# Performance work log

Measured on AMD Instinct MI355X. Metric: run time of the kernel, lower is better.

The kernel has to match this reference:

```python
import jax, jax.numpy as jnp
import numpy as np

B, S, HID = 2, 2048, 2048
NH, HD = 16, 128
QR, KR, VR = 6, 2, 2
SCALING = HD ** -0.5


def _rope_factors(x, cos, sin):
    # x: [b, s, rank, hd]; cos/sin: [s, hd//2]
    half = x.shape[-1] // 2
    x1, x2 = x[..., :half], x[..., half:]
    c = cos[None, :, None, :]
    s = sin[None, :, None, :]
    return jnp.concatenate([x1 * c - x2 * s, x1 * s + x2 * c], axis=-1)


def setup_inputs() -> dict:
    key = jax.random.key(0)
    ks = jax.random.split(key, 9)
    hidden_states = jax.random.normal(ks[0], (B, S, HID), dtype=jnp.float32)
    # proper RoPE frequencies
    inv_freq = 1.0 / (10000.0 ** (np.arange(0, HD, 2, dtype=np.float32) / HD))
    ang = np.arange(S, dtype=np.float32)[:, None] * inv_freq[None, :]  # [S, HD//2]
    freqs_cos = jnp.asarray(np.cos(ang), dtype=jnp.float32)
    freqs_sin = jnp.asarray(np.sin(ang), dtype=jnp.float32)
    kv_write_indices = jnp.arange(S, dtype=jnp.int64 if jax.config.jax_enable_x64 else jnp.int32)
    mask = jnp.zeros((B, 1, S, S), dtype=jnp.float32)
    sc = 0.02
    W_A_q = jax.random.normal(ks[1], (NH * QR, HID), dtype=jnp.float32) * sc
    W_A_k = jax.random.normal(ks[2], (NH * KR, HID), dtype=jnp.float32) * sc
    W_A_v = jax.random.normal(ks[3], (NH * VR, HID), dtype=jnp.float32) * sc
    W_B_q = jax.random.normal(ks[4], (QR * HD, HID), dtype=jnp.float32) * sc
    W_B_k = jax.random.normal(ks[5], (KR * HD, HID), dtype=jnp.float32) * sc
    W_B_v = jax.random.normal(ks[6], (VR * HD, HID), dtype=jnp.float32) * sc
    W_o = jax.random.normal(ks[7], (HID, NH * HD), dtype=jnp.float32) * sc
    return dict(hidden_states=hidden_states, freqs_cos=freqs_cos, freqs_sin=freqs_sin,
                kv_write_indices=kv_write_indices, mask=mask,
                W_A_q=W_A_q, W_A_k=W_A_k, W_A_v=W_A_v,
                W_B_q=W_B_q, W_B_k=W_B_k, W_B_v=W_B_v, W_o=W_o)


def reference(hidden_states, freqs_cos, freqs_sin, kv_write_indices, mask,
              W_A_q, W_A_k, W_A_v, W_B_q, W_B_k, W_B_v, W_o):
    b, s, _ = hidden_states.shape
    x = hidden_states
    # low-rank factor projections (torch Linear: x @ W.T)
    A_q = (x @ W_A_q.T).reshape(b, s, NH, QR)
    A_k = (x @ W_A_k.T).reshape(b, s, NH, KR)
    A_v = (x @ W_A_v.T).reshape(b, s, NH, VR)
    B_q = (x @ W_B_q.T).reshape(b, s, QR, HD)
    B_k = (x @ W_B_k.T).reshape(b, s, KR, HD)
    B_v = (x @ W_B_v.T).reshape(b, s, VR, HD)
    # per-rank RoPE on B factors of q and k (vectorized over rank)
    B_q = _rope_factors(B_q, freqs_cos, freqs_sin)
    B_k = _rope_factors(B_k, freqs_cos, freqs_sin)
    # kv_write_indices == arange(s): cache is fully overwritten, so current
    # activations are the full KV state (prefill).
    # reconstruct q/k/v from factor pairs
    q = jnp.einsum('bshr,bsrd->bshd', A_q, B_q) / QR
    k = jnp.einsum('bshr,bsrd->bshd', A_k, B_k) / KR
    v = jnp.einsum('bshr,bsrd->bshd', A_v, B_v) / VR
    # attention: [b, h, q, k]
    scores = jnp.einsum('bqhd,bkhd->bhqk', q * SCALING, k)
    scores = scores + mask
    probs = jax.nn.softmax(scores.astype(jnp.float32), axis=-1).astype(q.dtype)
    out = jnp.einsum('bhqk,bkhd->bqhd', probs, v).reshape(b, s, NH * HD)
    return out @ W_o.T
```

## Files before the change

### kernel.cpp

```cpp
#include <hip/hip_runtime.h>


typedef __attribute__((ext_vector_type(8))) __bf16 bf16x8;
typedef __attribute__((ext_vector_type(4))) float f32x4;

__device__ __forceinline__ unsigned short f2bf(float f) {
  union { float f; unsigned u; } v; v.f = f;
  unsigned u = v.u;
  u += 0x7fffu + ((u >> 16) & 1u);
  return (unsigned short)(u >> 16);
}

__device__ __forceinline__ void glds16(const void* g, void* l) {
  __builtin_amdgcn_global_load_lds(
      (const __attribute__((address_space(1))) void*)g,
      (__attribute__((address_space(3))) void*)l, 16, 0, 0);
}

__global__ void cast_bf16_k(const float* __restrict__ src,
                            unsigned short* __restrict__ dst, int n4) {
  int i = blockIdx.x * 256 + threadIdx.x;
  if (i < n4) {
    float4 f = reinterpret_cast<const float4*>(src)[i];
    ushort4 o;
    o.x = f2bf(f.x); o.y = f2bf(f.y); o.z = f2bf(f.z); o.w = f2bf(f.w);
    reinterpret_cast<ushort4*>(dst)[i] = o;
  }
}

__global__ __launch_bounds__(256, 2) void gemm_bt(
    const unsigned short* __restrict__ A, const unsigned short* __restrict__ Bt,
    float* __restrict__ C, int M, int N, int K) {
  __shared__ __align__(16) unsigned short As[128 * 32];
  __shared__ __align__(16) unsigned short Bs[128 * 32];
  const int tid = threadIdx.x;
  const int lane = tid & 63, wave = tid >> 6;
  const int l15 = lane & 15, quad = lane >> 4;
  const long bm = (long)blockIdx.y * 128, bn = (long)blockIdx.x * 128;
  const int wm = (wave >> 1) * 64, wn = (wave & 1) * 64;
  const f32x4 zero4 = {0.f, 0.f, 0.f, 0.f};
  f32x4 acc[4][4];
#pragma unroll
  for (int i = 0; i < 4; i++)
#pragma unroll
    for (int j = 0; j < 4; j++) acc[i][j] = zero4;

  const int g0 = tid, g1 = tid + 256;
  for (int k0 = 0; k0 < K; k0 += 32) {
    glds16(A + (bm + (g0 >> 2)) * K + k0 + (g0 & 3) * 8, As + g0 * 8);
    glds16(A + (bm + (g1 >> 2)) * K + k0 + (g1 & 3) * 8, As + g1 * 8);
    glds16(Bt + (bn + (g0 >> 2)) * K + k0 + (g0 & 3) * 8, Bs + g0 * 8);
    glds16(Bt + (bn + (g1 >> 2)) * K + k0 + (g1 & 3) * 8, Bs + g1 * 8);
    __syncthreads();
    bf16x8 af[4], bfr[4];
#pragma unroll
    for (int mi = 0; mi < 4; mi++)
      af[mi] = *(const bf16x8*)(As + (wm + mi * 16 + l15) * 32 + quad * 8);
#pragma unroll
    for (int ni = 0; ni < 4; ni++)
      bfr[ni] = *(const bf16x8*)(Bs + (wn + ni * 16 + l15) * 32 + quad * 8);
#pragma unroll
    for (int mi = 0; mi < 4; mi++)
#pragma unroll
      for (int ni = 0; ni < 4; ni++)
        acc[mi][ni] = __builtin_amdgcn_mfma_f32_16x16x32_bf16(
            af[mi], bfr[ni], acc[mi][ni], 0, 0, 0);
    __syncthreads();
  }
#pragma unroll
  for (int mi = 0; mi < 4; mi++)
#pragma unroll
    for (int ni = 0; ni < 4; ni++)
#pragma unroll
      for (int e = 0; e < 4; e++) {
        long r = bm + wm + mi * 16 + quad * 4 + e;
        long c = bn + wn + ni * 16 + l15;
        C[r * (long)N + c] = acc[mi][ni][e];
      }
}

__global__ __launch_bounds__(256) void rope_contract(
    const float* __restrict__ P, const float* __restrict__ cos_t,
    const float* __restrict__ sin_t, unsigned short* __restrict__ qo,
    unsigned short* __restrict__ ko, unsigned short* __restrict__ vo) {
  const int row = blockIdx.x;
  const int b = row >> 11, s = row & 2047;
  const float* p = P + (size_t)row * 1536;
  __shared__ float Af[160];
  __shared__ float Bqr[768], Bkr[256], Bvr[256];
  const int tid = threadIdx.x;
  if (tid < 160) Af[tid] = p[tid];
  for (int i = tid; i < 768; i += 256) {
    int r = i >> 7, d = i & 127;
    float out;
    if (d < 64) {
      float x1 = p[160 + r * 128 + d], x2 = p[160 + r * 128 + d + 64];
      out = x1 * cos_t[s * 64 + d] - x2 * sin_t[s * 64 + d];
    } else {
      int dd = d - 64;
      float x1 = p[160 + r * 128 + dd], x2 = p[160 + r * 128 + d];
      out = x1 * sin_t[s * 64 + dd] + x2 * cos_t[s * 64 + dd];
    }
    Bqr[i] = out;
  }
  {
    int i = tid;
    int r = i >> 7, d = i & 127;
    float out;
    if (d < 64) {
      float x1 = p[928 + r * 128 + d], x2 = p[928 + r * 128 + d + 64];
      out = x1 * cos_t[s * 64 + d] - x2 * sin_t[s * 64 + d];
    } else {
      int dd = d - 64;
      float x1 = p[928 + r * 128 + dd], x2 = p[928 + r * 128 + d];
      out = x1 * sin_t[s * 64 + dd] + x2 * cos_t[s * 64 + dd];
    }
    Bkr[i] = out;
    Bvr[i] = p[1184 + i];
  }
  __syncthreads();
  const float qscale = 0.08838834764831845f / 6.0f * 1.4426950408889634f;
  for (int i = tid; i < 2048; i += 256) {
    int h = i >> 7, d = i & 127;
    float aq = 0.f;
#pragma unroll
    for (int r = 0; r < 6; r++) aq += Af[h * 6 + r] * Bqr[r * 128 + d];
    float ak = Af[96 + h * 2] * Bkr[d] + Af[96 + h * 2 + 1] * Bkr[128 + d];
    float av = Af[128 + h * 2] * Bvr[d] + Af[128 + h * 2 + 1] * Bvr[128 + d];
    size_t o = ((size_t)(b * 16 + h) * 2048 + s) * 128 + d;
    qo[o] = f2bf(aq * qscale);
    ko[o] = f2bf(ak * 0.5f);
    vo[o] = f2bf(av * 0.5f);
  }
}

__global__ void transpose_v(const unsigned short* __restrict__ v,
                            unsigned short* __restrict__ vT) {
  __shared__ unsigned short t[32][33];
  const int bh = blockIdx.z, d0 = blockIdx.x * 32, s0 = blockIdx.y * 32;
  const int tx = threadIdx.x & 31, ty = threadIdx.x >> 5;
  const unsigned short* src = v + (size_t)bh * 2048 * 128;
  unsigned short* dst = vT + (size_t)bh * 128 * 2048;
#pragma unroll
  for (int j = 0; j < 32; j += 8)
    t[ty + j][tx] = src[(size_t)(s0 + ty + j) * 128 + d0 + tx];
  __syncthreads();
#pragma unroll
  for (int j = 0; j < 32; j += 8)
    dst[(size_t)(d0 + ty + j) * 2048 + s0 + tx] = t[tx][ty + j];
}

__global__ __launch_bounds__(512, 2) void attn_k(
    const unsigned short* __restrict__ q, const unsigned short* __restrict__ k,
    const unsigned short* __restrict__ vT, unsigned short* __restrict__ O) {
  const int bh = blockIdx.y;
  const int b = bh >> 4, h = bh & 15;
  const int q0 = blockIdx.x * 256;
  const int tid = threadIdx.x, wave = tid >> 6, lane = tid & 63;
  const int l15 = lane & 15, quad = lane >> 4;
  __shared__ __align__(16) unsigned short Kb[2][64 * 128];
  __shared__ __align__(16) unsigned short Vb[2][128 * 64];
  __shared__ __align__(16) unsigned short Ps[8][32 * 40];
  unsigned short* pw = &Ps[wave][0];
  const f32x4 zero4 = {0.f, 0.f, 0.f, 0.f};

  bf16x8 qf[2][4];
  {
    const unsigned short* qbase =
        q + ((size_t)bh * 2048 + q0 + wave * 32) * 128;
#pragma unroll
    for (int mi = 0; mi < 2; mi++)
#pragma unroll
      for (int ks = 0; ks < 4; ks++)
        qf[mi][ks] = *(const bf16x8*)(qbase + (size_t)(mi * 16 + l15) * 128 +
                                      ks * 32 + quad * 8);
  }
  bf16x8 ones;
#pragma unroll
  for (int i = 0; i < 8; i++) ones[i] = (__bf16)1.0f;

  f32x4 oacc[2][9];
#pragma unroll
  for (int mi = 0; mi < 2; mi++)
#pragma unroll
    for (int nd = 0; nd < 9; nd++) oacc[mi][nd] = zero4;

  const unsigned short* kg[2];
  const unsigned short* vg[2];
#pragma unroll
  for (int j = 0; j < 2; j++) {
    int t = tid + j * 512;
    int r = t >> 4, cb = (t & 15) ^ (r & 15);
    kg[j] = k + ((size_t)bh * 2048 + r) * 128 + cb * 8;
    int d = t >> 3, cv = (t & 7) ^ (d & 7);
    vg[j] = vT + ((size_t)bh * 128 + d) * 2048 + cv * 8;
  }

#define STAGE(KT, BUF)                                                        \
  {                                                                           \
    _Pragma("unroll") for (int j = 0; j < 2; j++) {                           \
      glds16(kg[j] + (size_t)(KT) * 128, &Kb[BUF][(tid + j * 512) * 8]);      \
      glds16(vg[j] + (KT), &Vb[BUF][(tid + j * 512) * 8]);                    \
    }                                                                         \
  }

  STAGE(0, 0);
  for (int it = 0; it < 32; it++) {
    __syncthreads();
    if (it + 1 < 32) STAGE((it + 1) * 64, (it + 1) & 1);
    const unsigned short* Kt = &Kb[it & 1][0];
    const unsigned short* Vt = &Vb[it & 1][0];

#pragma unroll
    for (int half = 0; half < 2; half++) {
      f32x4 sacc[2][2];
#pragma unroll
      for (int mi = 0; mi < 2; mi++) { sacc[mi][0] = zero4; sacc[mi][1] = zero4; }
#pragma unroll
      for (int ks = 0; ks < 4; ks++) {
        bf16x8 b0 = *(const bf16x8*)(
            Kt + (size_t)(half * 32 + l15) * 128 + (((ks * 4 + quad) ^ l15) * 8));
        bf16x8 b1 = *(const bf16x8*)(
            Kt + (size_t)(half * 32 + 16 + l15) * 128 + (((ks * 4 + quad) ^ l15) * 8));
#pragma unroll
        for (int mi = 0; mi < 2; mi++) {
          sacc[mi][0] = __builtin_amdgcn_mfma_f32_16x16x32_bf16(
              qf[mi][ks], b0, sacc[mi][0], 0, 0, 0);
          sacc[mi][1] = __builtin_amdgcn_mfma_f32_16x16x32_bf16(
              qf[mi][ks], b1, sacc[mi][1], 0, 0, 0);
        }
      }
#pragma unroll
      for (int mi = 0; mi < 2; mi++)
#pragma unroll
        for (int ni = 0; ni < 2; ni++)
#pragma unroll
          for (int e = 0; e < 4; e++) {
            float pv = __builtin_exp2f(sacc[mi][ni][e]);
            pw[(mi * 16 + quad * 4 + e) * 40 + ni * 16 + l15] =
                (unsigned short)(__float_as_uint(pv) >> 16);
          }
      bf16x8 bv[8];
#pragma unroll
      for (int nd = 0; nd < 8; nd++)
        bv[nd] = *(const bf16x8*)(
            Vt + (size_t)(nd * 16 + l15) * 64 + (((half * 4 + quad) ^ (l15 & 7)) * 8));
#pragma unroll
      for (int mi = 0; mi < 2; mi++) {
        bf16x8 af = *(const bf16x8*)(pw + (size_t)(mi * 16 + l15) * 40 + quad * 8);
#pragma unroll
        for (int nd = 0; nd < 8; nd++)
          oacc[mi][nd] = __builtin_amdgcn_mfma_f32_16x16x32_bf16(
              af, bv[nd], oacc[mi][nd], 0, 0, 0);
        oacc[mi][8] = __builtin_amdgcn_mfma_f32_16x16x32_bf16(
            af, ones, oacc[mi][8], 0, 0, 0);
      }
    }
  }

#pragma unroll
  for (int mi = 0; mi < 2; mi++)
#pragma unroll
    for (int e = 0; e < 4; e++) {
      float rl = 1.0f / oacc[mi][8][e];
      int srow = q0 + wave * 32 + mi * 16 + quad * 4 + e;
      size_t obase = ((size_t)b * 2048 + srow) * 2048 + h * 128;
#pragma unroll
      for (int nd = 0; nd < 8; nd++)
        O[obase + nd * 16 + l15] = f2bf(oacc[mi][nd][e] * rl);
    }
#undef STAGE
}

extern "C" void kernel_launch(void* const* d_in, const int* in_sizes, int n_in,
                              void* d_out, int out_size, void* d_ws, size_t ws_size,
                              hipStream_t stream) {
  const float* x   = (const float*)d_in[0];
  const float* fc  = (const float*)d_in[1];
  const float* fs  = (const float*)d_in[2];
  const float* WAq = (const float*)d_in[5];
  const float* WAk = (const float*)d_in[6];
  const float* WAv = (const float*)d_in[7];
  const float* WBq = (const float*)d_in[8];
  const float* WBk = (const float*)d_in[9];
  const float* WBv = (const float*)d_in[10];
  const float* Wo  = (const float*)d_in[11];
  float* out = (float*)d_out;
  char* ws = (char*)d_ws;

  unsigned short* Xbf  = (unsigned short*)(ws);
  unsigned short* Wcat = (unsigned short*)(ws + 16777216);
  unsigned short* Wob  = (unsigned short*)(ws + 23068672);
  float*          P    = (float*)(ws + 31457280);
  unsigned short* qb   = (unsigned short*)(ws + 56623104);
  unsigned short* kb   = (unsigned short*)(ws + 73400320);
  unsigned short* vb   = (unsigned short*)(ws + 90177536);
  unsigned short* vT   = Xbf;
  unsigned short* Ob   = (unsigned short*)P;

  auto cast = [&](const float* s, unsigned short* d, int n) {
    int n4 = n >> 2;
    cast_bf16_k<<<(n4 + 255) / 256, 256, 0, stream>>>(s, d, n4);
  };
  cast(x,   Xbf,               2 * 2048 * 2048);
  cast(WAq, Wcat + 0 * 2048,   96 * 2048);
  cast(WAk, Wcat + 96 * 2048,  32 * 2048);
  cast(WAv, Wcat + 128 * 2048, 32 * 2048);
  cast(WBq, Wcat + 160 * 2048, 768 * 2048);
  cast(WBk, Wcat + 928 * 2048, 256 * 2048);
  cast(WBv, Wcat + 1184 * 2048, 256 * 2048);
  cast(Wo,  Wob,               2048 * 2048);
  hipMemsetAsync(Wcat + 1440 * 2048, 0, (1536 - 1440) * 2048 * sizeof(unsigned short), stream);

  gemm_bt<<<dim3(12, 32), 256, 0, stream>>>(Xbf, Wcat, P, 4096, 1536, 2048);
  rope_contract<<<4096, 256, 0, stream>>>(P, fc, fs, qb, kb, vb);
  transpose_v<<<dim3(4, 64, 32), 256, 0, stream>>>(vb, vT);
  attn_k<<<dim3(8, 32), 512, 0, stream>>>(qb, kb, vT, Ob);
  gemm_bt<<<dim3(16, 32), 256, 0, stream>>>(Ob, Wob, out, 4096, 2048, 2048);
}
```

Baseline: 368.7 us.

## Fuse casts into one kernel and retile attention to 128-row blocks

Folds the eight cast launches and the memset into one kernel that picks its source and destination by index range, removing launch overhead. The attention kernel moves to 256-thread blocks covering 128 query rows, which doubles the grid to 512 blocks for better CU fill on 256 CUs. Block IDs are swizzled so that consecutive blocks go to different (b,h) pairs, and s_setprio raises wave priority around the MFMA sections. Smaller blocks mean each block re-stages the full K/V for fewer queries, so total K/V load traffic grows.

Result: faster. 344.7 us (-6.5%).

```diff
diff --git a/kernel.cpp b/kernel.cpp
--- a/kernel.cpp
+++ b/kernel.cpp
@@ -17,15 +17,32 @@
       (__attribute__((address_space(3))) void*)l, 16, 0, 0);
 }
 
-__global__ void cast_bf16_k(const float* __restrict__ src,
-                            unsigned short* __restrict__ dst, int n4) {
+__global__ __launch_bounds__(256) void cast_all_k(
+    const float* __restrict__ x, const float* __restrict__ WAq,
+    const float* __restrict__ WAk, const float* __restrict__ WAv,
+    const float* __restrict__ WBq, const float* __restrict__ WBk,
+    const float* __restrict__ WBv, const float* __restrict__ Wo,
+    unsigned short* __restrict__ Xbf, unsigned short* __restrict__ Wcat,
+    unsigned short* __restrict__ Wob) {
   int i = blockIdx.x * 256 + threadIdx.x;
-  if (i < n4) {
-    float4 f = reinterpret_cast<const float4*>(src)[i];
-    ushort4 o;
-    o.x = f2bf(f.x); o.y = f2bf(f.y); o.z = f2bf(f.z); o.w = f2bf(f.w);
-    reinterpret_cast<ushort4*>(dst)[i] = o;
-  }
+  const float* src; unsigned short* dst; int r;
+  if (i < 2097152)      { src = x;   dst = Xbf;               r = i; }
+  else if (i < 2146304) { src = WAq; dst = Wcat;              r = i - 2097152; }
+  else if (i < 2162688) { src = WAk; dst = Wcat + 96 * 2048;  r = i - 2146304; }
+  else if (i < 2179072) { src = WAv; dst = Wcat + 128 * 2048; r = i - 2162688; }
+  else if (i < 2572288) { src = WBq; dst = Wcat + 160 * 2048; r = i - 2179072; }
+  else if (i < 2703360) { src = WBk; dst = Wcat + 928 * 2048; r = i - 2572288; }
+  else if (i < 2834432) { src = WBv; dst = Wcat + 1184 * 2048; r = i - 2703360; }
+  else if (i < 3883008) { src = Wo;  dst = Wob;               r = i - 2834432; }
+  else {
+    ushort4 z = {0, 0, 0, 0};
+    reinterpret_cast<ushort4*>(Wcat + 1440 * 2048)[i - 3883008] = z;
+    return;
+  }
+  float4 f = reinterpret_cast<const float4*>(src)[r];
+  ushort4 o;
+  o.x = f2bf(f.x); o.y = f2bf(f.y); o.z = f2bf(f.z); o.w = f2bf(f.w);
+  reinterpret_cast<ushort4*>(dst)[r] = o;
 }
 
 __global__ __launch_bounds__(256, 2) void gemm_bt(
@@ -150,17 +167,19 @@
     dst[(size_t)(d0 + ty + j) * 2048 + s0 + tx] = t[tx][ty + j];
 }
 
-__global__ __launch_bounds__(512, 2) void attn_k(
+__global__ __launch_bounds__(256, 2) void attn_k(
     const unsigned short* __restrict__ q, const unsigned short* __restrict__ k,
     const unsigned short* __restrict__ vT, unsigned short* __restrict__ O) {
-  const int bh = blockIdx.y;
+  const int orig = blockIdx.y * 16 + blockIdx.x;
+  const int swz = (orig & 7) * 64 + (orig >> 3);
+  const int bh = swz >> 4;
   const int b = bh >> 4, h = bh & 15;
-  const int q0 = blockIdx.x * 256;
+  const int q0 = (swz & 15) * 128;
   const int tid = threadIdx.x, wave = tid >> 6, lane = tid & 63;
   const int l15 = lane & 15, quad = lane >> 4;
   __shared__ __align__(16) unsigned short Kb[2][64 * 128];
   __shared__ __align__(16) unsigned short Vb[2][128 * 64];
-  __shared__ __align__(16) unsigned short Ps[8][32 * 40];
+  __shared__ __align__(16) unsigned short Ps[4][32 * 40];
   unsigned short* pw = &Ps[wave][0];
   const f32x4 zero4 = {0.f, 0.f, 0.f, 0.f};
 
@@ -185,11 +204,11 @@
 #pragma unroll
     for (int nd = 0; nd < 9; nd++) oacc[mi][nd] = zero4;
 
-  const unsigned short* kg[2];
-  const unsigned short* vg[2];
-#pragma unroll
-  for (int j = 0; j < 2; j++) {
-    int t = tid + j * 512;
+  const unsigned short* kg[4];
+  const unsigned short* vg[4];
+#pragma unroll
+  for (int j = 0; j < 4; j++) {
+    int t = tid + j * 256;
     int r = t >> 4, cb = (t & 15) ^ (r & 15);
     kg[j] = k + ((size_t)bh * 2048 + r) * 128 + cb * 8;
     int d = t >> 3, cv = (t & 7) ^ (d & 7);
@@ -198,9 +217,9 @@
 
 #define STAGE(KT, BUF)                                                        \
   {                                                                           \
-    _Pragma("unroll") for (int j = 0; j < 2; j++) {                           \
-      glds16(kg[j] + (size_t)(KT) * 128, &Kb[BUF][(tid + j * 512) * 8]);      \
-      glds16(vg[j] + (KT), &Vb[BUF][(tid + j * 512) * 8]);                    \
+    _Pragma("unroll") for (int j = 0; j < 4; j++) {                           \
+      glds16(kg[j] + (size_t)(KT) * 128, &Kb[BUF][(tid + j * 256) * 8]);      \
+      glds16(vg[j] + (KT), &Vb[BUF][(tid + j * 256) * 8]);                    \
     }                                                                         \
   }
 
@@ -216,6 +235,7 @@
       f32x4 sacc[2][2];
 #pragma unroll
       for (int mi = 0; mi < 2; mi++) { sacc[mi][0] = zero4; sacc[mi][1] = zero4; }
+      __builtin_amdgcn_s_setprio(1);
 #pragma unroll
       for (int ks = 0; ks < 4; ks++) {
         bf16x8 b0 = *(const bf16x8*)(
@@ -230,6 +250,7 @@
               qf[mi][ks], b1, sacc[mi][1], 0, 0, 0);
         }
       }
+      __builtin_amdgcn_s_setprio(0);
 #pragma unroll
       for (int mi = 0; mi < 2; mi++)
 #pragma unroll
@@ -245,6 +266,7 @@
       for (int nd = 0; nd < 8; nd++)
         bv[nd] = *(const bf16x8*)(
             Vt + (size_t)(nd * 16 + l15) * 64 + (((half * 4 + quad) ^ (l15 & 7)) * 8));
+      __builtin_amdgcn_s_setprio(1);
 #pragma unroll
       for (int mi = 0; mi < 2; mi++) {
         bf16x8 af = *(const bf16x8*)(pw + (size_t)(mi * 16 + l15) * 40 + quad * 8);
@@ -255,6 +277,7 @@
         oacc[mi][8] = __builtin_amdgcn_mfma_f32_16x16x32_bf16(
             af, ones, oacc[mi][8], 0, 0, 0);
       }
+      __builtin_amdgcn_s_setprio(0);
     }
   }
 
@@ -298,23 +321,12 @@
   unsigned short* vT   = Xbf;
   unsigned short* Ob   = (unsigned short*)P;
 
-  auto cast = [&](const float* s, unsigned short* d, int n) {
-    int n4 = n >> 2;
-    cast_bf16_k<<<(n4 + 255) / 256, 256, 0, stream>>>(s, d, n4);
-  };
-  cast(x,   Xbf,               2 * 2048 * 2048);
-  cast(WAq, Wcat + 0 * 2048,   96 * 2048);
-  cast(WAk, Wcat + 96 * 2048,  32 * 2048);
-  cast(WAv, Wcat + 128 * 2048, 32 * 2048);
-  cast(WBq, Wcat + 160 * 2048, 768 * 2048);
-  cast(WBk, Wcat + 928 * 2048, 256 * 2048);
-  cast(WBv, Wcat + 1184 * 2048, 256 * 2048);
-  cast(Wo,  Wob,               2048 * 2048);
-  hipMemsetAsync(Wcat + 1440 * 2048, 0, (1536 - 1440) * 2048 * sizeof(unsigned short), stream);
+  cast_all_k<<<15360, 256, 0, stream>>>(x, WAq, WAk, WAv, WBq, WBk, WBv, Wo,
+                                        Xbf, Wcat, Wob);
 
   gemm_bt<<<dim3(12, 32), 256, 0, stream>>>(Xbf, Wcat, P, 4096, 1536, 2048);
   rope_contract<<<4096, 256, 0, stream>>>(P, fc, fs, qb, kb, vb);
   transpose_v<<<dim3(4, 64, 32), 256, 0, stream>>>(vb, vT);
-  attn_k<<<dim3(8, 32), 512, 0, stream>>>(qb, kb, vT, Ob);
+  attn_k<<<dim3(16, 32), 256, 0, stream>>>(qb, kb, vT, Ob);
   gemm_bt<<<dim3(16, 32), 256, 0, stream>>>(Ob, Wob, out, 4096, 2048, 2048);
 }
```
